# Optimization experiments

Measured on AMD Instinct MI355X. Metric: run time of the kernel, lower is better.

Reference implementation:

```python
import jax, jax.numpy as jnp
import numpy as np

N, E, D, H1, H2 = 50000, 800000, 128, 128, 128


def setup_inputs() -> dict:
    key = jax.random.key(0)
    ks = jax.random.split(key, 9)
    s = 0.05
    return {
        "x": jax.random.normal(ks[0], (N, D), dtype=jnp.float32),
        "edge_index": jax.random.randint(ks[1], (2, E), 0, N, dtype=jnp.int64),
        "W_l1": jax.random.normal(ks[2], (D, H1), dtype=jnp.float32) * s,
        "b_l1": jnp.zeros((H1,), dtype=jnp.float32),
        "W_r1": jax.random.normal(ks[3], (D, H1), dtype=jnp.float32) * s,
        "W_l2": jax.random.normal(ks[4], (H1, H2), dtype=jnp.float32) * s,
        "b_l2": jnp.zeros((H2,), dtype=jnp.float32),
        "W_r2": jax.random.normal(ks[5], (H1, H2), dtype=jnp.float32) * s,
        "W_e": jax.random.normal(ks[6], (2 * H2, 1), dtype=jnp.float32) * s,
        "b_e": jnp.zeros((1,), dtype=jnp.float32),
    }


def _sage_conv(h, src, tgt, n_nodes, W_l, b_l, W_r):
    # PyG SAGEConv (mean aggr): out = lin_l(mean_{j in N(i)} h_j) + lin_r(h_i)
    msg = h[src]                                              # [E, F] gather
    agg = jax.ops.segment_sum(msg, tgt, num_segments=n_nodes)  # [N, F]
    cnt = jax.ops.segment_sum(jnp.ones((src.shape[0], 1), h.dtype), tgt,
                              num_segments=n_nodes)            # [N, 1]
    mean = agg / jnp.maximum(cnt, 1.0)                         # empty nbrs -> 0
    return mean @ W_l + b_l + h @ W_r


def reference(x, edge_index, W_l1, b_l1, W_r1, W_l2, b_l2, W_r2, W_e, b_e):
    src, tgt = edge_index[0], edge_index[1]
    n_nodes = x.shape[0]
    h = jax.nn.relu(_sage_conv(x, src, tgt, n_nodes, W_l1, b_l1, W_r1))
    # dropout is identity in eval mode
    h = _sage_conv(h, src, tgt, n_nodes, W_l2, b_l2, W_r2)
    z = jnp.concatenate([h[src], h[tgt]], axis=-1)  # [E, 2*H2]
    y = z @ W_e + b_e                                # [E, 1]
    return jax.nn.sigmoid(y)
```

## Files before the change

### kernel.cpp

```cpp
#include <hip/hip_runtime.h>

#define NN 50000
#define NE 800000
#define DD 128
#define BUCKETS 196
#define PB 4096
#define PBLK 196
#define EMAX 6144
#define BPAD 264
#define PACKB 6250

typedef unsigned int uint_t;
typedef unsigned short ush_t;
typedef __attribute__((ext_vector_type(8))) short short8;
typedef __attribute__((ext_vector_type(4))) float f32x4;

__device__ __forceinline__ float bflo(uint_t u) { return __uint_as_float(u << 16); }
__device__ __forceinline__ float bfhi(uint_t u) { return __uint_as_float(u & 0xffff0000u); }
__device__ __forceinline__ ush_t f2bf(float f) {
  uint_t u = __float_as_uint(f);
  u += 0x7fffu + ((u >> 16) & 1u);
  return (ush_t)(u >> 16);
}
__device__ __forceinline__ uint_t pack2(float a, float b) {
  return (uint_t)f2bf(a) | ((uint_t)f2bf(b) << 16);
}

__device__ __forceinline__ int ld_idx(const void* ei, int is64, long long i) {
  return is64 ? (int)((const long long*)ei)[i] : ((const int*)ei)[i];
}

__device__ __forceinline__ int detect64(const void* ei) {
  const unsigned long long* p = (const unsigned long long*)ei;
  unsigned long long w = p[threadIdx.x & 63];
  return __ballot((w >> 32) != 0) == 0ull ? 1 : 0;
}

__device__ __forceinline__ int block_incl_scan(int v, int tid, int* wsum) {
  int lane = tid & 63, wave = tid >> 6;
  int s = v;
#pragma unroll
  for (int off = 1; off < 64; off <<= 1) {
    int u = __shfl_up(s, off, 64);
    if (lane >= off) s += u;
  }
  if (lane == 63) wsum[wave] = s;
  __syncthreads();
  int base = 0;
  if (wave > 0) base += wsum[0];
  if (wave > 1) base += wsum[1];
  if (wave > 2) base += wsum[2];
  return base + s;
}

__global__ __launch_bounds__(256) void prep_part_k(
    const void* __restrict__ ei, int* __restrict__ bcur,
    uint_t* __restrict__ pbuf, uint_t* __restrict__ epk,
    const float* __restrict__ x, ush_t* __restrict__ xb,
    const float* __restrict__ Wl1, const float* __restrict__ Wr1,
    const float* __restrict__ Wl2, const float* __restrict__ Wr2,
    ush_t* __restrict__ Wt1, ush_t* __restrict__ Wt2) {
  __shared__ int hist[256];
  __shared__ int basel[256];
  __shared__ int cur[256];
  __shared__ int gbase[256];
  __shared__ int wsum[4];
  __shared__ uint_t buf[PB];
  __shared__ unsigned char bbuf[PB];
  int tid = threadIdx.x;
  int blk = blockIdx.x;
  if (blk >= PBLK) {
    blk -= PBLK;
    if (blk < PACKB) {
      int i = blk * 256 + tid;
      float4 v = reinterpret_cast<const float4*>(x)[i];
      uint2 o;
      o.x = pack2(v.x, v.y);
      o.y = pack2(v.z, v.w);
      reinterpret_cast<uint2*>(xb)[i] = o;
      return;
    }
    blk -= PACKB;
    int e = blk * 256 + tid;
    int layer = e >> 15;
    int r = e & 32767;
    int col = r >> 8;
    int k = r & 255;
    const float* Wl = layer ? Wl2 : Wl1;
    const float* Wr = layer ? Wr2 : Wr1;
    float v = (k < DD) ? Wl[k * DD + col] : Wr[(k - DD) * DD + col];
    ush_t* Wt = layer ? Wt2 : Wt1;
    Wt[col * 256 + k] = f2bf(v);
    return;
  }
  int is64 = detect64(ei);
  hist[tid] = 0;
  __syncthreads();
  long long base = (long long)blk * PB;
  uint_t pv[PB / 256];
#pragma unroll
  for (int i = 0; i < PB / 256; ++i) {
    long long e = base + i * 256 + tid;
    if (e < NE) {
      int s = ld_idx(ei, is64, e);
      int d = ld_idx(ei, is64, (long long)NE + e);
      pv[i] = ((uint_t)(d >> 8) << 24) | ((uint_t)(d & 255) << 16) | (uint_t)s;
      epk[e] = ((uint_t)d << 16) | (uint_t)s;
      atomicAdd(&hist[d >> 8], 1);
    } else {
      pv[i] = 0xFFFFFFFFu;
    }
  }
  __syncthreads();
  int hv = hist[tid];
  int incl = block_incl_scan(hv, tid, wsum);
  basel[tid] = incl - hv;
  cur[tid] = incl - hv;
  if (hv > 0) gbase[tid] = atomicAdd(&bcur[tid], hv);
  __syncthreads();
#pragma unroll
  for (int i = 0; i < PB / 256; ++i) {
    uint_t p = pv[i];
    if (p != 0xFFFFFFFFu) {
      int b = p >> 24;
      int r = atomicAdd(&cur[b], 1);
      buf[r] = p & 0xFFFFFFu;
      bbuf[r] = (unsigned char)b;
    }
  }
  __syncthreads();
  int total = basel[255] + hist[255];
  for (int j = tid; j < total; j += 256) {
    int b = bbuf[j];
    int slot = gbase[b] + (j - basel[b]);
    if (slot < EMAX) pbuf[(size_t)b * EMAX + slot] = buf[j];
  }
}

__global__ __launch_bounds__(256) void csr_k(const uint_t* __restrict__ pbuf,
                                             const int* __restrict__ bcur,
                                             int* __restrict__ offsets,
                                             int* __restrict__ srclist) {
  __shared__ int cnt[256];
  __shared__ int scur[256];
  __shared__ int wsum[4];
  __shared__ int sgb, scnt, stot;
  __shared__ uint_t ebuf[EMAX];
  int tid = threadIdx.x;
  int b = blockIdx.x;
  int v = 0;
  if (tid < BUCKETS) {
    v = bcur[tid];
    if (v > EMAX) v = EMAX;
  }
  int incl = block_incl_scan(v, tid, wsum);
  if (tid == b) { sgb = incl - v; scnt = v; }
  if (tid == BUCKETS - 1) stot = incl;
  cnt[tid] = 0;
  __syncthreads();
  int gb = sgb;
  int ecnt = scnt;
  for (int j = tid; j < ecnt; j += 256) {
    uint_t e = pbuf[(size_t)b * EMAX + j];
    ebuf[j] = e;
    atomicAdd(&cnt[(e >> 16) & 255], 1);
  }
  __syncthreads();
  int c = cnt[tid];
  int incl2 = block_incl_scan(c, tid, wsum);
  int ex = incl2 - c;
  scur[tid] = ex;
  int node = b * 256 + tid;
  if (node < NN) offsets[node] = gb + ex;
  if (b == BUCKETS - 1 && tid == 0) offsets[NN] = stot;
  __syncthreads();
  for (int j = tid; j < ecnt; j += 256) {
    uint_t e = ebuf[j];
    int p = atomicAdd(&scur[(e >> 16) & 255], 1);
    srclist[gb + p] = (int)(e & 0xFFFFu);
  }
}

__global__ __launch_bounds__(256) void agg_k(const ush_t* __restrict__ featb,
                                             const int* __restrict__ srclist,
                                             const int* __restrict__ offsets,
                                             ush_t* __restrict__ meanb) {
  int t = blockIdx.x * 256 + threadIdx.x;
  int node = t >> 4;
  int lane = t & 15;
  int f = lane << 3;
  int beg = offsets[node];
  int end = offsets[node + 1];
  float a0 = 0.f, a1 = 0.f, a2 = 0.f, a3 = 0.f, a4 = 0.f, a5 = 0.f, a6 = 0.f, a7 = 0.f;
  for (int c = beg; c < end; c += 16) {
    int idx = c + lane;
    int sl = (idx < end) ? srclist[idx] : 0;
    int m = min(16, end - c);
    int jj = 0;
    for (; jj + 4 <= m; jj += 4) {
      int s0 = __shfl(sl, jj, 16);
      int s1 = __shfl(sl, jj + 1, 16);
      int s2 = __shfl(sl, jj + 2, 16);
      int s3 = __shfl(sl, jj + 3, 16);
      uint4 v0 = *reinterpret_cast<const uint4*>(featb + (size_t)s0 * DD + f);
      uint4 v1 = *reinterpret_cast<const uint4*>(featb + (size_t)s1 * DD + f);
      uint4 v2 = *reinterpret_cast<const uint4*>(featb + (size_t)s2 * DD + f);
      uint4 v3 = *reinterpret_cast<const uint4*>(featb + (size_t)s3 * DD + f);
      a0 += bflo(v0.x); a1 += bfhi(v0.x); a2 += bflo(v0.y); a3 += bfhi(v0.y);
      a4 += bflo(v0.z); a5 += bfhi(v0.z); a6 += bflo(v0.w); a7 += bfhi(v0.w);
      a0 += bflo(v1.x); a1 += bfhi(v1.x); a2 += bflo(v1.y); a3 += bfhi(v1.y);
      a4 += bflo(v1.z); a5 += bfhi(v1.z); a6 += bflo(v1.w); a7 += bfhi(v1.w);
      a0 += bflo(v2.x); a1 += bfhi(v2.x); a2 += bflo(v2.y); a3 += bfhi(v2.y);
      a4 += bflo(v2.z); a5 += bfhi(v2.z); a6 += bflo(v2.w); a7 += bfhi(v2.w);
      a0 += bflo(v3.x); a1 += bfhi(v3.x); a2 += bflo(v3.y); a3 += bfhi(v3.y);
      a4 += bflo(v3.z); a5 += bfhi(v3.z); a6 += bflo(v3.w); a7 += bfhi(v3.w);
    }
    for (; jj < m; ++jj) {
      int s = __shfl(sl, jj, 16);
      uint4 v = *reinterpret_cast<const uint4*>(featb + (size_t)s * DD + f);
      a0 += bflo(v.x); a1 += bfhi(v.x); a2 += bflo(v.y); a3 += bfhi(v.y);
      a4 += bflo(v.z); a5 += bfhi(v.z); a6 += bflo(v.w); a7 += bfhi(v.w);
    }
  }
  float inv = 1.0f / fmaxf((float)(end - beg), 1.0f);
  uint4 o;
  o.x = pack2(a0 * inv, a1 * inv);
  o.y = pack2(a2 * inv, a3 * inv);
  o.z = pack2(a4 * inv, a5 * inv);
  o.w = pack2(a6 * inv, a7 * inv);
  *reinterpret_cast<uint4*>(meanb + (size_t)node * DD + f) = o;
}

#define MFMA_CORE(A0PTR, A1PTR, WTPTR)                                         \
  int tid = threadIdx.x;                                                       \
  int lane = tid & 63;                                                         \
  int wave = tid >> 6;                                                         \
  int n15 = lane & 15, quad = lane >> 4;                                       \
  int nb = blockIdx.x * 64;                                                    \
  for (int it = 0; it < 16; ++it) {                                            \
    int i = it * 256 + tid;                                                    \
    int col = i >> 5, c = i & 31;                                              \
    *reinterpret_cast<short8*>(&sB[col * BPAD + c * 8]) =                      \
        reinterpret_cast<const short8*>(WTPTR)[i];                             \
  }                                                                            \
  __syncthreads();                                                             \
  int row = nb + wave * 16 + n15;                                              \
  int arow = (row < NN) ? row : (NN - 1);                                      \
  const ush_t* a0 = A0PTR + (size_t)arow * DD;                                 \
  const ush_t* a1 = A1PTR + (size_t)arow * DD;                                 \
  f32x4 acc[8];                                                                \
  _Pragma("unroll")                                                            \
  for (int t = 0; t < 8; ++t) acc[t] = (f32x4){0.f, 0.f, 0.f, 0.f};           \
  _Pragma("unroll")                                                            \
  for (int c = 0; c < 8; ++c) {                                                \
    const ush_t* ap = (c < 4) ? (a0 + c * 32 + quad * 8)                       \
                              : (a1 + (c - 4) * 32 + quad * 8);                \
    short8 af = *reinterpret_cast<const short8*>(ap);                          \
    int kb = c * 32 + quad * 8;                                                \
    _Pragma("unroll")                                                          \
    for (int t = 0; t < 8; ++t) {                                              \
      short8 bf = *reinterpret_cast<const short8*>(&sB[(t * 16 + n15) * BPAD + kb]); \
      acc[t] = __builtin_amdgcn_mfma_f32_16x16x32_bf16(af, bf, acc[t], 0, 0, 0); \
    }                                                                          \
  }

__global__ __launch_bounds__(256, 2) void sage_l1(
    const ush_t* __restrict__ meanb, const ush_t* __restrict__ xb,
    const ush_t* __restrict__ Wt1, const float* __restrict__ bl,
    ush_t* __restrict__ h1b) {
  __shared__ ush_t sB[128 * BPAD];
  MFMA_CORE(meanb, xb, Wt1)
#pragma unroll
  for (int t = 0; t < 8; ++t) {
    int col = t * 16 + n15;
    float b = bl[col];
#pragma unroll
    for (int reg = 0; reg < 4; ++reg) {
      int r = nb + wave * 16 + quad * 4 + reg;
      if (r < NN)
        h1b[(size_t)r * DD + col] = f2bf(fmaxf(acc[t][reg] + b, 0.f));
    }
  }
}

__global__ __launch_bounds__(256, 2) void sage_l2(
    const ush_t* __restrict__ meanb, const ush_t* __restrict__ h1b,
    const ush_t* __restrict__ Wt2, const float* __restrict__ bl,
    const float* __restrict__ We, float2* __restrict__ s12) {
  __shared__ ush_t sB[128 * BPAD];
  MFMA_CORE(meanb, h1b, Wt2)
  float p1[4] = {0.f, 0.f, 0.f, 0.f};
  float p2[4] = {0.f, 0.f, 0.f, 0.f};
#pragma unroll
  for (int t = 0; t < 8; ++t) {
    int col = t * 16 + n15;
    float b = bl[col];
    float w1 = We[col];
    float w2 = We[DD + col];
#pragma unroll
    for (int reg = 0; reg < 4; ++reg) {
      float v = acc[t][reg] + b;
      p1[reg] += v * w1;
      p2[reg] += v * w2;
    }
  }
#pragma unroll
  for (int reg = 0; reg < 4; ++reg) {
    float v1 = p1[reg], v2 = p2[reg];
    for (int off = 8; off > 0; off >>= 1) {
      v1 += __shfl_down(v1, off, 16);
      v2 += __shfl_down(v2, off, 16);
    }
    int r = nb + wave * 16 + quad * 4 + reg;
    if (n15 == 0 && r < NN) s12[r] = make_float2(v1, v2);
  }
}

__global__ __launch_bounds__(256) void edge_k(const uint_t* __restrict__ epk,
                                              const float2* __restrict__ s12,
                                              const float* __restrict__ be,
                                              float* __restrict__ out) {
  int e = blockIdx.x * 256 + threadIdx.x;
  uint_t p = epk[e];
  float2 a = s12[p & 0xFFFFu];
  float2 b = s12[p >> 16];
  float v = a.x + b.y + be[0];
  out[e] = 1.0f / (1.0f + __expf(-v));
}

extern "C" void kernel_launch(void* const* d_in, const int* in_sizes, int n_in,
                              void* d_out, int out_size, void* d_ws, size_t ws_size,
                              hipStream_t stream) {
  const float* x   = (const float*)d_in[0];
  const void*  ei  = d_in[1];
  const float* Wl1 = (const float*)d_in[2];
  const float* bl1 = (const float*)d_in[3];
  const float* Wr1 = (const float*)d_in[4];
  const float* Wl2 = (const float*)d_in[5];
  const float* bl2 = (const float*)d_in[6];
  const float* Wr2 = (const float*)d_in[7];
  const float* We  = (const float*)d_in[8];
  const float* be  = (const float*)d_in[9];
  float* out = (float*)d_out;

  int* bcur    = (int*)d_ws;
  int* offsets = bcur + 256;
  uint_t* epk  = (uint_t*)(offsets + 50004);
  uint_t* pbuf = epk + NE;
  int* srclist = (int*)(pbuf + (size_t)BUCKETS * EMAX);
  ush_t* xb    = (ush_t*)(srclist + NE);
  ush_t* meanb = xb + (size_t)NN * DD;
  ush_t* h1b   = meanb + (size_t)NN * DD;
  float2* s12  = (float2*)(h1b + (size_t)NN * DD);
  ush_t* Wt1   = (ush_t*)((float*)s12 + 2 * NN);
  ush_t* Wt2   = Wt1 + 32768;

  hipMemsetAsync(bcur, 0, 256 * sizeof(int), stream);
  prep_part_k<<<PBLK + PACKB + 256, 256, 0, stream>>>(
      ei, bcur, pbuf, epk, x, xb, Wl1, Wr1, Wl2, Wr2, Wt1, Wt2);
  csr_k<<<BUCKETS, 256, 0, stream>>>(pbuf, bcur, offsets, srclist);

  int gemm_blocks = (NN + 63) / 64;
  agg_k<<<(NN * 16) / 256, 256, 0, stream>>>(xb, srclist, offsets, meanb);
  sage_l1<<<gemm_blocks, 256, 0, stream>>>(meanb, xb, Wt1, bl1, h1b);

  agg_k<<<(NN * 16) / 256, 256, 0, stream>>>(h1b, srclist, offsets, meanb);
  sage_l2<<<gemm_blocks, 256, 0, stream>>>(meanb, h1b, Wt2, bl2, We, s12);

  edge_k<<<NE / 256, 256, 0, stream>>>(epk, s12, be, out);
}
```

Baseline: 221.7 us.

## Fold layer-2 linear maps and edge projection into per-node scalars

Since layer 2 is linear and is followed by a linear edge projection, the change precomputes W_l2·We and W_r2·We vectors and a bias constant. Layer 1's epilogue then emits four per-node scalars instead of a bf16 hidden matrix. This removes the second 128-wide aggregation and the second MFMA GEMM, replacing them with a two-float neighbor mean. Rounding changes slightly because h1 is no longer quantized to bf16.

```diff
diff --git a/kernel.cpp b/kernel.cpp
--- a/kernel.cpp
+++ b/kernel.cpp
@@ -9,6 +9,7 @@
 #define EMAX 6144
 #define BPAD 264
 #define PACKB 6250
+#define WTB 128
 
 typedef unsigned int uint_t;
 typedef unsigned short ush_t;
@@ -59,7 +60,9 @@
     const float* __restrict__ x, ush_t* __restrict__ xb,
     const float* __restrict__ Wl1, const float* __restrict__ Wr1,
     const float* __restrict__ Wl2, const float* __restrict__ Wr2,
-    ush_t* __restrict__ Wt1, ush_t* __restrict__ Wt2) {
+    const float* __restrict__ We, const float* __restrict__ bl2,
+    const float* __restrict__ be,
+    ush_t* __restrict__ Wt1, float* __restrict__ uv, float* __restrict__ cc) {
   __shared__ int hist[256];
   __shared__ int basel[256];
   __shared__ int cur[256];
@@ -70,9 +73,44 @@
   int tid = threadIdx.x;
   int blk = blockIdx.x;
   if (blk >= PBLK) {
-    blk -= PBLK;
-    if (blk < PACKB) {
-      int i = blk * 256 + tid;
+    int blk2 = blk - PBLK;
+    if (blk2 < 2) {
+      const float* W = blk2 ? Wr2 : Wl2;
+      int base = blk2 * 256;
+      int wave = tid >> 6, lane = tid & 63;
+      float e0 = We[lane], e1 = We[64 + lane];
+      float f0 = We[128 + lane], f1 = We[192 + lane];
+      for (int k = wave * 32; k < wave * 32 + 32; ++k) {
+        float m0 = W[k * DD + lane];
+        float m1 = W[k * DD + 64 + lane];
+        float p = m0 * e0 + m1 * e1;
+        float q = m0 * f0 + m1 * f1;
+#pragma unroll
+        for (int off = 32; off > 0; off >>= 1) {
+          p += __shfl_down(p, off, 64);
+          q += __shfl_down(q, off, 64);
+        }
+        if (lane == 0) {
+          uv[base + k] = p;
+          uv[base + 128 + k] = q;
+        }
+      }
+      return;
+    }
+    if (blk2 == 2) {
+      if (tid < 64) {
+        int k = tid;
+        float p = bl2[k] * (We[k] + We[128 + k]) +
+                  bl2[k + 64] * (We[k + 64] + We[192 + k]);
+#pragma unroll
+        for (int off = 32; off > 0; off >>= 1) p += __shfl_down(p, off, 64);
+        if (k == 0) cc[0] = p + be[0];
+      }
+      return;
+    }
+    blk2 -= 3;
+    if (blk2 < PACKB) {
+      int i = blk2 * 256 + tid;
       float4 v = reinterpret_cast<const float4*>(x)[i];
       uint2 o;
       o.x = pack2(v.x, v.y);
@@ -80,17 +118,12 @@
       reinterpret_cast<uint2*>(xb)[i] = o;
       return;
     }
-    blk -= PACKB;
-    int e = blk * 256 + tid;
-    int layer = e >> 15;
-    int r = e & 32767;
-    int col = r >> 8;
-    int k = r & 255;
-    const float* Wl = layer ? Wl2 : Wl1;
-    const float* Wr = layer ? Wr2 : Wr1;
-    float v = (k < DD) ? Wl[k * DD + col] : Wr[(k - DD) * DD + col];
-    ush_t* Wt = layer ? Wt2 : Wt1;
-    Wt[col * 256 + k] = f2bf(v);
+    blk2 -= PACKB;
+    int e = blk2 * 256 + tid;
+    int col = e >> 8;
+    int k = e & 255;
+    float v = (k < DD) ? Wl1[k * DD + col] : Wr1[(k - DD) * DD + col];
+    Wt1[col * 256 + k] = f2bf(v);
     return;
   }
   int is64 = detect64(ei);
@@ -267,64 +300,85 @@
 __global__ __launch_bounds__(256, 2) void sage_l1(
     const ush_t* __restrict__ meanb, const ush_t* __restrict__ xb,
     const ush_t* __restrict__ Wt1, const float* __restrict__ bl,
-    ush_t* __restrict__ h1b) {
+    const float* __restrict__ uv, float2* __restrict__ t12,
+    float2* __restrict__ r12) {
   __shared__ ush_t sB[128 * BPAD];
   MFMA_CORE(meanb, xb, Wt1)
+  float p1[4] = {0.f, 0.f, 0.f, 0.f};
+  float p2[4] = {0.f, 0.f, 0.f, 0.f};
+  float q1[4] = {0.f, 0.f, 0.f, 0.f};
+  float q2[4] = {0.f, 0.f, 0.f, 0.f};
 #pragma unroll
   for (int t = 0; t < 8; ++t) {
     int col = t * 16 + n15;
     float b = bl[col];
+    float U1 = uv[col];
+    float U2 = uv[128 + col];
+    float V1 = uv[256 + col];
+    float V2 = uv[384 + col];
 #pragma unroll
     for (int reg = 0; reg < 4; ++reg) {
-      int r = nb + wave * 16 + quad * 4 + reg;
-      if (r < NN)
-        h1b[(size_t)r * DD + col] = f2bf(fmaxf(acc[t][reg] + b, 0.f));
-    }
-  }
-}
-
-__global__ __launch_bounds__(256, 2) void sage_l2(
-    const ush_t* __restrict__ meanb, const ush_t* __restrict__ h1b,
-    const ush_t* __restrict__ Wt2, const float* __restrict__ bl,
-    const float* __restrict__ We, float2* __restrict__ s12) {
-  __shared__ ush_t sB[128 * BPAD];
-  MFMA_CORE(meanb, h1b, Wt2)
-  float p1[4] = {0.f, 0.f, 0.f, 0.f};
-  float p2[4] = {0.f, 0.f, 0.f, 0.f};
-#pragma unroll
-  for (int t = 0; t < 8; ++t) {
-    int col = t * 16 + n15;
-    float b = bl[col];
-    float w1 = We[col];
-    float w2 = We[DD + col];
-#pragma unroll
-    for (int reg = 0; reg < 4; ++reg) {
-      float v = acc[t][reg] + b;
-      p1[reg] += v * w1;
-      p2[reg] += v * w2;
+      float h = fmaxf(acc[t][reg] + b, 0.f);
+      p1[reg] += h * U1;
+      p2[reg] += h * U2;
+      q1[reg] += h * V1;
+      q2[reg] += h * V2;
     }
   }
 #pragma unroll
   for (int reg = 0; reg < 4; ++reg) {
-    float v1 = p1[reg], v2 = p2[reg];
+    float a1 = p1[reg], a2 = p2[reg], b1 = q1[reg], b2 = q2[reg];
     for (int off = 8; off > 0; off >>= 1) {
-      v1 += __shfl_down(v1, off, 16);
-      v2 += __shfl_down(v2, off, 16);
+      a1 += __shfl_down(a1, off, 16);
+      a2 += __shfl_down(a2, off, 16);
+      b1 += __shfl_down(b1, off, 16);
+      b2 += __shfl_down(b2, off, 16);
     }
     int r = nb + wave * 16 + quad * 4 + reg;
-    if (n15 == 0 && r < NN) s12[r] = make_float2(v1, v2);
+    if (n15 == 0 && r < NN) {
+      t12[r] = make_float2(a1, a2);
+      r12[r] = make_float2(b1, b2);
+    }
+  }
+}
+
+__global__ __launch_bounds__(256) void agg2s_k(const float2* __restrict__ t12,
+                                               const int* __restrict__ srclist,
+                                               const int* __restrict__ offsets,
+                                               const float2* __restrict__ r12,
+                                               float2* __restrict__ s12) {
+  int t = blockIdx.x * 256 + threadIdx.x;
+  int node = t >> 4;
+  int lane = t & 15;
+  int beg = offsets[node];
+  int end = offsets[node + 1];
+  float sx = 0.f, sy = 0.f;
+  for (int c = beg + lane; c < end; c += 16) {
+    int s = srclist[c];
+    float2 v = t12[s];
+    sx += v.x;
+    sy += v.y;
+  }
+  for (int off = 8; off > 0; off >>= 1) {
+    sx += __shfl_down(sx, off, 16);
+    sy += __shfl_down(sy, off, 16);
+  }
+  if (lane == 0) {
+    float inv = 1.0f / fmaxf((float)(end - beg), 1.0f);
+    float2 r = r12[node];
+    s12[node] = make_float2(sx * inv + r.x, sy * inv + r.y);
   }
 }
 
 __global__ __launch_bounds__(256) void edge_k(const uint_t* __restrict__ epk,
                                               const float2* __restrict__ s12,
-                                              const float* __restrict__ be,
+                                              const float* __restrict__ cc,
                                               float* __restrict__ out) {
   int e = blockIdx.x * 256 + threadIdx.x;
   uint_t p = epk[e];
   float2 a = s12[p & 0xFFFFu];
   float2 b = s12[p >> 16];
-  float v = a.x + b.y + be[0];
+  float v = a.x + b.y + cc[0];
   out[e] = 1.0f / (1.0f + __expf(-v));
 }
 
@@ -350,22 +404,24 @@
   int* srclist = (int*)(pbuf + (size_t)BUCKETS * EMAX);
   ush_t* xb    = (ush_t*)(srclist + NE);
   ush_t* meanb = xb + (size_t)NN * DD;
-  ush_t* h1b   = meanb + (size_t)NN * DD;
-  float2* s12  = (float2*)(h1b + (size_t)NN * DD);
-  ush_t* Wt1   = (ush_t*)((float*)s12 + 2 * NN);
-  ush_t* Wt2   = Wt1 + 32768;
+  float2* t12  = (float2*)(meanb + (size_t)NN * DD);
+  float2* r12  = t12 + NN;
+  float2* s12  = r12 + NN;
+  ush_t* Wt1   = (ush_t*)(s12 + NN);
+  float* uv    = (float*)(Wt1 + 32768);
+  float* cc    = uv + 512;
 
   hipMemsetAsync(bcur, 0, 256 * sizeof(int), stream);
-  prep_part_k<<<PBLK + PACKB + 256, 256, 0, stream>>>(
-      ei, bcur, pbuf, epk, x, xb, Wl1, Wr1, Wl2, Wr2, Wt1, Wt2);
+  prep_part_k<<<PBLK + 3 + PACKB + WTB, 256, 0, stream>>>(
+      ei, bcur, pbuf, epk, x, xb, Wl1, Wr1, Wl2, Wr2, We, bl2, be, Wt1, uv, cc);
   csr_k<<<BUCKETS, 256, 0, stream>>>(pbuf, bcur, offsets, srclist);
 
+  agg_k<<<(NN * 16) / 256, 256, 0, stream>>>(xb, srclist, offsets, meanb);
+
   int gemm_blocks = (NN + 63) / 64;
-  agg_k<<<(NN * 16) / 256, 256, 0, stream>>>(xb, srclist, offsets, meanb);
-  sage_l1<<<gemm_blocks, 256, 0, stream>>>(meanb, xb, Wt1, bl1, h1b);
-
-  agg_k<<<(NN * 16) / 256, 256, 0, stream>>>(h1b, srclist, offsets, meanb);
-  sage_l2<<<gemm_blocks, 256, 0, stream>>>(meanb, h1b, Wt2, bl2, We, s12);
-
-  edge_k<<<NE / 256, 256, 0, stream>>>(epk, s12, be, out);
-}
+  sage_l1<<<gemm_blocks, 256, 0, stream>>>(meanb, xb, Wt1, bl1, uv, t12, r12);
+
+  agg2s_k<<<(NN * 16) / 256, 256, 0, stream>>>(t12, srclist, offsets, r12, s12);
+
+  edge_k<<<NE / 256, 256, 0, stream>>>(epk, s12, cc, out);
+}
```

Measured after the change: 183.3 us. -17.3%, faster.
